# Optimization experiments

Measured on AMD Instinct MI355X. Metric: run time of the kernel, lower is better.

## Reference

```python
import jax, jax.numpy as jnp
import numpy as np

T = 2048      # tokens
H = 1024      # hidden_size
HQ = 16       # num query heads
HK = 4        # num kv heads
D = 64        # head_dim
E = 8         # num experts
K = 2         # top_k
I = 2048      # expert intermediate size
EPS = 1e-5
THETA = 10000.0


def setup_inputs() -> dict:
    key = jax.random.key(0)
    ks = jax.random.split(key, 8)
    s = 0.02
    return {
        "hidden_states": jax.random.normal(ks[0], (T, H), jnp.float32),
        "positions": jnp.arange(T, dtype=jnp.int32),
        "qkv_w": jax.random.normal(ks[1], ((HQ + 2 * HK) * D, H), jnp.float32) * s,
        "o_w": jax.random.normal(ks[2], (H, HQ * D), jnp.float32) * s,
        "norm_in_w": jnp.ones((H,), jnp.float32),
        "norm_post_w": jnp.ones((H,), jnp.float32),
        "norm_next_w": jnp.ones((H,), jnp.float32),
        "gate_w": jax.random.normal(ks[3], (E, H), jnp.float32) * s,
        "w1": jax.random.normal(ks[4], (E, I, H), jnp.float32) * s,
        "w3": jax.random.normal(ks[5], (E, I, H), jnp.float32) * s,
        "w2": jax.random.normal(ks[6], (E, H, I), jnp.float32) * s,
    }


def rmsnorm(x, w):
    var = jnp.mean(x * x, axis=-1, keepdims=True)
    return x * jax.lax.rsqrt(var + EPS) * w


def rope_neox(x, positions):
    # x: [T, nH, D]; rotate-half (neox) style
    half = D // 2
    inv_freq = 1.0 / (THETA ** (jnp.arange(0, half, dtype=jnp.float32) * 2.0 / D))
    ang = positions.astype(jnp.float32)[:, None] * inv_freq[None, :]      # [T, D/2]
    cos = jnp.cos(ang)[:, None, :]
    sin = jnp.sin(ang)[:, None, :]
    x1, x2 = x[..., :half], x[..., half:]
    return jnp.concatenate([x1 * cos - x2 * sin, x2 * cos + x1 * sin], axis=-1)


def reference(hidden_states, positions, qkv_w, o_w, norm_in_w, norm_post_w,
              norm_next_w, gate_w, w1, w3, w2):
    x = hidden_states                               # [T, H]
    residual = x
    h = rmsnorm(x, norm_in_w)                       # input_layernorm

    # ---- attention (GQA, causal, neox RoPE) ----
    qkv = h @ qkv_w.T                               # [T, (HQ+2HK)*D]
    q, k, v = jnp.split(qkv, [HQ * D, (HQ + HK) * D], axis=-1)
    q = rope_neox(q.reshape(T, HQ, D), positions)
    k = rope_neox(k.reshape(T, HK, D), positions)
    v = v.reshape(T, HK, D)
    rep = HQ // HK
    k = jnp.repeat(k, rep, axis=1)                  # [T, HQ, D]
    v = jnp.repeat(v, rep, axis=1)
    scale = D ** -0.5
    scores = jnp.einsum('qhd,khd->hqk', q, k) * scale   # [HQ, T, T]
    mask = jnp.tril(jnp.ones((T, T), dtype=bool))
    scores = jnp.where(mask[None], scores, -jnp.inf)
    probs = jax.nn.softmax(scores, axis=-1)
    attn = jnp.einsum('hqk,khd->qhd', probs, v).reshape(T, HQ * D)
    attn_out = attn @ o_w.T                         # [T, H]

    # fused allreduce(identity, world=1) + residual add + post_attention RMSNorm
    residual = residual + attn_out
    h = rmsnorm(residual, norm_post_w)

    # ---- MoE: gate, top-2, renormalize, SiLU-gated experts ----
    logits = h @ gate_w.T                           # [T, E]
    route = jax.nn.softmax(logits, axis=-1)
    topw, topi = jax.lax.top_k(route, K)            # [T, K]
    topw = topw / jnp.sum(topw, axis=-1, keepdims=True)   # renormalize
    # dense combine weights [T, E] (zero for unselected experts)
    wdense = jnp.sum(jax.nn.one_hot(topi, E, dtype=h.dtype) * topw[..., None], axis=1)
    h1 = jnp.einsum('td,eid->tei', h, w1)           # [T, E, I]
    h3 = jnp.einsum('td,eid->tei', h, w3)
    gated = jax.nn.silu(h1) * h3
    moe_out = jnp.einsum('tei,edi,te->td', gated, w2, wdense)   # [T, H]

    # fused allreduce(identity) + residual add + next layer norm
    residual = residual + moe_out
    h = rmsnorm(residual, norm_next_w)
    return h
```

## Files before the change

### kernel.cpp

```cpp
#include <hip/hip_runtime.h>
#include <hip/hip_bf16.h>
#include <math.h>

#define T_ 2048
#define H_ 1024
#define HQ_ 16
#define HK_ 4
#define D_ 64
#define NE_ 8
#define II_ 2048

typedef __attribute__((ext_vector_type(8))) short bf16x8;
typedef __attribute__((ext_vector_type(8))) unsigned short u16x8;
typedef __attribute__((ext_vector_type(4))) float f32x4;

#define GLOAD16(g, l)                                                                   \
  __builtin_amdgcn_global_load_lds((const __attribute__((address_space(1))) unsigned int*)(g), \
                                   (__attribute__((address_space(3))) unsigned int*)(l), 16, 0, 0)

__device__ __forceinline__ unsigned short f2bf(float f) {
  unsigned int u = __float_as_uint(f);
  return (unsigned short)((u + 0x7fffu + ((u >> 16) & 1u)) >> 16);
}
__device__ __forceinline__ float bf2f(unsigned short h) {
  return __uint_as_float((unsigned int)h << 16);
}

__global__ __launch_bounds__(256) void k_rmsnorm(const float* __restrict__ x, const float* __restrict__ w,
                                                 float* __restrict__ outf, unsigned short* __restrict__ outb) {
  int row = blockIdx.x;
  int tid = threadIdx.x;
  float4 v = ((const float4*)(x + (size_t)row * H_))[tid];
  float ss = v.x * v.x + v.y * v.y + v.z * v.z + v.w * v.w;
#pragma unroll
  for (int off = 32; off; off >>= 1) ss += __shfl_xor(ss, off, 64);
  __shared__ float red[4];
  int lane = tid & 63, wid = tid >> 6;
  if (lane == 0) red[wid] = ss;
  __syncthreads();
  float tot = red[0] + red[1] + red[2] + red[3];
  float inv = rsqrtf(tot * (1.0f / H_) + 1e-5f);
  float4 wv = ((const float4*)w)[tid];
  float4 o;
  o.x = v.x * inv * wv.x; o.y = v.y * inv * wv.y; o.z = v.z * inv * wv.z; o.w = v.w * inv * wv.w;
  ((float4*)(outf + (size_t)row * H_))[tid] = o;
  if (outb) {
    ushort4 b; b.x = f2bf(o.x); b.y = f2bf(o.y); b.z = f2bf(o.z); b.w = f2bf(o.w);
    ((ushort4*)(outb + (size_t)row * H_))[tid] = b;
  }
}

__global__ __launch_bounds__(256) void k_rmsnorm_split(const float* __restrict__ x, const float* __restrict__ w,
                                                       unsigned short* __restrict__ Aq) {
  int row = blockIdx.x;
  int tid = threadIdx.x;
  float4 v = ((const float4*)(x + (size_t)row * H_))[tid];
  float ss = v.x * v.x + v.y * v.y + v.z * v.z + v.w * v.w;
#pragma unroll
  for (int off = 32; off; off >>= 1) ss += __shfl_xor(ss, off, 64);
  __shared__ float red[4];
  int lane = tid & 63, wid = tid >> 6;
  if (lane == 0) red[wid] = ss;
  __syncthreads();
  float tot = red[0] + red[1] + red[2] + red[3];
  float inv = rsqrtf(tot * (1.0f / H_) + 1e-5f);
  float4 wv = ((const float4*)w)[tid];
  float4 o;
  o.x = v.x * inv * wv.x; o.y = v.y * inv * wv.y; o.z = v.z * inv * wv.z; o.w = v.w * inv * wv.w;
  ushort4 hi, lo;
  hi.x = f2bf(o.x); hi.y = f2bf(o.y); hi.z = f2bf(o.z); hi.w = f2bf(o.w);
  lo.x = f2bf(o.x - bf2f(hi.x)); lo.y = f2bf(o.y - bf2f(hi.y));
  lo.z = f2bf(o.z - bf2f(hi.z)); lo.w = f2bf(o.w - bf2f(hi.w));
  size_t base = (size_t)row * (3 * H_) + tid * 4;
  *(ushort4*)(Aq + base) = hi;
  *(ushort4*)(Aq + base + H_) = hi;
  *(ushort4*)(Aq + base + 2 * H_) = lo;
}

__global__ __launch_bounds__(256) void k_wsplit(const float* __restrict__ in, unsigned short* __restrict__ out,
                                                int K, int n8total) {
  int stride = gridDim.x * 256;
  int kc8 = K >> 3;
  for (int i = blockIdx.x * 256 + threadIdx.x; i < n8total; i += stride) {
    int n = i / kc8, kc = (i - n * kc8) * 8;
    const float4* p = (const float4*)(in + (size_t)n * K + kc);
    float4 a = p[0], b = p[1];
    u16x8 hi, lo;
    hi[0] = f2bf(a.x); hi[1] = f2bf(a.y); hi[2] = f2bf(a.z); hi[3] = f2bf(a.w);
    hi[4] = f2bf(b.x); hi[5] = f2bf(b.y); hi[6] = f2bf(b.z); hi[7] = f2bf(b.w);
    lo[0] = f2bf(a.x - bf2f(hi[0])); lo[1] = f2bf(a.y - bf2f(hi[1]));
    lo[2] = f2bf(a.z - bf2f(hi[2])); lo[3] = f2bf(a.w - bf2f(hi[3]));
    lo[4] = f2bf(b.x - bf2f(hi[4])); lo[5] = f2bf(b.y - bf2f(hi[5]));
    lo[6] = f2bf(b.z - bf2f(hi[6])); lo[7] = f2bf(b.w - bf2f(hi[7]));
    size_t ob = (size_t)n * 3 * K + kc;
    *(u16x8*)(out + ob) = hi;
    *(u16x8*)(out + ob + K) = lo;
    *(u16x8*)(out + ob + 2 * K) = hi;
  }
}

template <int ADD>
__global__ __launch_bounds__(256) void k_hgemm(const unsigned short* __restrict__ A, const unsigned short* __restrict__ B,
                                               float* __restrict__ C, const float* __restrict__ addsrc,
                                               int N, int K3) {
  int m0 = blockIdx.y * 128, n0 = blockIdx.x * 64;
  __shared__ unsigned short As[2][128 * 32];
  __shared__ unsigned short Bs[2][64 * 32];
  int tid = threadIdx.x, lane = tid & 63, w = tid >> 6;
  int wr = w >> 1, wc = w & 1;
  int l15 = lane & 15, lg = lane >> 4;
  int srow = lane >> 2, schunk = lane & 3;

  const unsigned short* ga0 = A + (size_t)(m0 + w * 32 + srow) * K3 + schunk * 8;
  const unsigned short* ga1 = A + (size_t)(m0 + w * 32 + 16 + srow) * K3 + schunk * 8;
  const unsigned short* gb = B + (size_t)(n0 + w * 16 + srow) * K3 + schunk * 8;

  f32x4 acc[4][2];
  f32x4 z = {0.f, 0.f, 0.f, 0.f};
#pragma unroll
  for (int a = 0; a < 4; a++)
#pragma unroll
    for (int b = 0; b < 2; b++) acc[a][b] = z;

  GLOAD16(ga0, &As[0][(w * 32) * 32]);
  GLOAD16(ga1, &As[0][(w * 32 + 16) * 32]);
  GLOAD16(gb, &Bs[0][(w * 16) * 32]);
  __syncthreads();

  int nt = K3 / 32;
  for (int t = 0; t < nt; ++t) {
    int cur = t & 1;
    if (t + 1 < nt) {
      int ko = (t + 1) * 32;
      GLOAD16(ga0 + ko, &As[cur ^ 1][(w * 32) * 32]);
      GLOAD16(ga1 + ko, &As[cur ^ 1][(w * 32 + 16) * 32]);
      GLOAD16(gb + ko, &Bs[cur ^ 1][(w * 16) * 32]);
    }
    bf16x8 af[4], bw2[2];
#pragma unroll
    for (int fa = 0; fa < 4; fa++)
      af[fa] = *(const bf16x8*)&As[cur][(wr * 64 + fa * 16 + l15) * 32 + lg * 8];
#pragma unroll
    for (int fb = 0; fb < 2; fb++)
      bw2[fb] = *(const bf16x8*)&Bs[cur][(wc * 32 + fb * 16 + l15) * 32 + lg * 8];
#pragma unroll
    for (int fa = 0; fa < 4; fa++)
#pragma unroll
      for (int fb = 0; fb < 2; fb++)
        acc[fa][fb] = __builtin_amdgcn_mfma_f32_16x16x32_bf16(af[fa], bw2[fb], acc[fa][fb], 0, 0, 0);
    __syncthreads();
  }
#pragma unroll
  for (int fa = 0; fa < 4; fa++)
#pragma unroll
    for (int r = 0; r < 4; r++) {
      int row = m0 + wr * 64 + fa * 16 + lg * 4 + r;
#pragma unroll
      for (int fb = 0; fb < 2; fb++) {
        int col = n0 + wc * 32 + fb * 16 + l15;
        float v = acc[fa][fb][r];
        if (ADD) v += addsrc[(size_t)row * N + col];
        C[(size_t)row * N + col] = v;
      }
    }
}

__global__ __launch_bounds__(256) void k_rope_table(const int* __restrict__ pos, float* __restrict__ ct,
                                                    float* __restrict__ st) {
  int idx = blockIdx.x * 256 + threadIdx.x;
  int t = idx >> 5, i = idx & 31;
  float p = (float)pow(10000.0, (double)i / 32.0);
  float freq = 1.0f / p;
  float ang = (float)pos[t] * freq;
  ct[idx] = cosf(ang);
  st[idx] = sinf(ang);
}

__global__ __launch_bounds__(256) void k_rope_prep(const float* __restrict__ qkv, const float* __restrict__ ct,
                                                   const float* __restrict__ st, unsigned short* __restrict__ Qhi,
                                                   unsigned short* __restrict__ Qlo, unsigned short* __restrict__ Khi,
                                                   unsigned short* __restrict__ Klo) {
  int t = blockIdx.x, tid = threadIdx.x;
  const float* row = qkv + (size_t)t * 1536;
#pragma unroll 2
  for (int it = tid; it < 512; it += 256) {
    int h = it >> 5, i = it & 31;
    float c = ct[t * 32 + i], s = st[t * 32 + i];
    float x1 = row[h * 64 + i], x2 = row[h * 64 + i + 32];
    float a = (x1 * c - x2 * s) * 0.125f;
    float b = (x2 * c + x1 * s) * 0.125f;
    size_t base = ((size_t)h * T_ + t) * 64 + i;
    unsigned short ah = f2bf(a), bh = f2bf(b);
    Qhi[base] = ah; Qhi[base + 32] = bh;
    Qlo[base] = f2bf(a - bf2f(ah));
    Qlo[base + 32] = f2bf(b - bf2f(bh));
  }
  if (tid < 128) {
    int h = tid >> 5, i = tid & 31;
    float c = ct[t * 32 + i], s = st[t * 32 + i];
    float x1 = row[1024 + h * 64 + i], x2 = row[1024 + h * 64 + i + 32];
    float a = x1 * c - x2 * s;
    float b = x2 * c + x1 * s;
    size_t base = ((size_t)h * T_ + t) * 64 + i;
    unsigned short ah = f2bf(a), bh = f2bf(b);
    Khi[base] = ah; Khi[base + 32] = bh;
    Klo[base] = f2bf(a - bf2f(ah));
    Klo[base + 32] = f2bf(b - bf2f(bh));
  }
}

__global__ __launch_bounds__(256) void k_vtrans(const float* __restrict__ qkv, unsigned short* __restrict__ Vthi,
                                                unsigned short* __restrict__ Vtlo) {
  int t0 = blockIdx.x * 64, h = blockIdx.y;
  __shared__ float tile[64][65];
  int tid = threadIdx.x;
  int c = tid & 63, w = tid >> 6;
  for (int r = w; r < 64; r += 4)
    tile[r][c] = qkv[(size_t)(t0 + r) * 1536 + 1280 + h * 64 + c];
  __syncthreads();
  for (int d = w; d < 64; d += 4) {
    float v = tile[c][d];
    unsigned short hi = f2bf(v);
    size_t idx = ((size_t)h * 64 + d) * T_ + t0 + c;
    Vthi[idx] = hi;
    Vtlo[idx] = f2bf(v - bf2f(hi));
  }
}

__global__ __launch_bounds__(256) void k_attn_mfma(const unsigned short* __restrict__ Qhi,
                                                   const unsigned short* __restrict__ Qlo,
                                                   const unsigned short* __restrict__ Khi,
                                                   const unsigned short* __restrict__ Klo,
                                                   const unsigned short* __restrict__ Vthi,
                                                   const unsigned short* __restrict__ Vtlo,
                                                   unsigned short* __restrict__ Ao) {
  int bid = blockIdx.x;
  int kk = bid >> 4;
  int head = bid & 15;
  int qidx = (kk < 16) ? (31 - kk) : (kk - 16);
  int qb = qidx * 64;
  int kvh = head >> 2;
  int tid = threadIdx.x, lane = tid & 63, w = tid >> 6;
  int l15 = lane & 15, lg = lane >> 4;

  __shared__ unsigned short KsH[64 * 72], KsL[64 * 72];
  __shared__ unsigned short VsH[64 * 72], VsL[64 * 72];
  __shared__ unsigned short PsH[64 * 72], PsL[64 * 72];

  bf16x8 qh[2], ql[2];
  {
    size_t qbase = ((size_t)head * T_ + qb + w * 16 + l15) * 64 + lg * 8;
    qh[0] = *(const bf16x8*)(Qhi + qbase);
    qh[1] = *(const bf16x8*)(Qhi + qbase + 32);
    ql[0] = *(const bf16x8*)(Qlo + qbase);
    ql[1] = *(const bf16x8*)(Qlo + qbase + 32);
  }
  f32x4 z = {0.f, 0.f, 0.f, 0.f};
  f32x4 Oa[4];
  float mrow[4], lrow[4];
#pragma unroll
  for (int r = 0; r < 4; r++) { mrow[r] = -1e30f; lrow[r] = 0.f; }
#pragma unroll
  for (int dg = 0; dg < 4; dg++) Oa[dg] = z;

  for (int jb = 0; jb <= qb; jb += 64) {
    __syncthreads();
    for (int c = tid; c < 512; c += 256) {
      int r = c >> 3, g = (c & 7) * 8;
      size_t kgl = ((size_t)kvh * T_ + jb + r) * 64 + g;
      size_t vgl = ((size_t)kvh * 64 + r) * T_ + jb + g;
      *(uint4*)&KsH[r * 72 + g] = *(const uint4*)(Khi + kgl);
      *(uint4*)&KsL[r * 72 + g] = *(const uint4*)(Klo + kgl);
      *(uint4*)&VsH[r * 72 + g] = *(const uint4*)(Vthi + vgl);
      *(uint4*)&VsL[r * 72 + g] = *(const uint4*)(Vtlo + vgl);
    }
    __syncthreads();

    f32x4 sc[4];
    sc[0] = z; sc[1] = z; sc[2] = z; sc[3] = z;
#pragma unroll
    for (int kg = 0; kg < 4; kg++) {
      int ba = (kg * 16 + l15) * 72 + lg * 8;
      bf16x8 bh0 = *(const bf16x8*)&KsH[ba];
      bf16x8 bh1 = *(const bf16x8*)&KsH[ba + 32];
      bf16x8 bl0 = *(const bf16x8*)&KsL[ba];
      bf16x8 bl1 = *(const bf16x8*)&KsL[ba + 32];
      sc[kg] = __builtin_amdgcn_mfma_f32_16x16x32_bf16(qh[0], bh0, sc[kg], 0, 0, 0);
      sc[kg] = __builtin_amdgcn_mfma_f32_16x16x32_bf16(qh[1], bh1, sc[kg], 0, 0, 0);
      sc[kg] = __builtin_amdgcn_mfma_f32_16x16x32_bf16(qh[0], bl0, sc[kg], 0, 0, 0);
      sc[kg] = __builtin_amdgcn_mfma_f32_16x16x32_bf16(qh[1], bl1, sc[kg], 0, 0, 0);
      sc[kg] = __builtin_amdgcn_mfma_f32_16x16x32_bf16(ql[0], bh0, sc[kg], 0, 0, 0);
      sc[kg] = __builtin_amdgcn_mfma_f32_16x16x32_bf16(ql[1], bh1, sc[kg], 0, 0, 0);
    }
    if (jb == qb) {
      int rb = w * 16 + lg * 4;
#pragma unroll
      for (int kg = 0; kg < 4; kg++) {
        int col = kg * 16 + l15;
#pragma unroll
        for (int r = 0; r < 4; r++)
          if (col > rb + r) sc[kg][r] = -1e30f;
      }
    }
#pragma unroll
    for (int r = 0; r < 4; r++) {
      float mt = fmaxf(fmaxf(sc[0][r], sc[1][r]), fmaxf(sc[2][r], sc[3][r]));
      mt = fmaxf(mt, __shfl_xor(mt, 1, 64));
      mt = fmaxf(mt, __shfl_xor(mt, 2, 64));
      mt = fmaxf(mt, __shfl_xor(mt, 4, 64));
      mt = fmaxf(mt, __shfl_xor(mt, 8, 64));
      float mnew = fmaxf(mrow[r], mt);
      float corr = __expf(mrow[r] - mnew);
      mrow[r] = mnew;
      float s = 0.f;
#pragma unroll
      for (int kg = 0; kg < 4; kg++) {
        float p = __expf(sc[kg][r] - mnew);
        sc[kg][r] = p;
        s += p;
      }
      s += __shfl_xor(s, 1, 64);
      s += __shfl_xor(s, 2, 64);
      s += __shfl_xor(s, 4, 64);
      s += __shfl_xor(s, 8, 64);
      lrow[r] = lrow[r] * corr + s;
#pragma unroll
      for (int dg = 0; dg < 4; dg++) Oa[dg][r] *= corr;
    }
    {
      int rb = w * 16 + lg * 4;
#pragma unroll
      for (int kg = 0; kg < 4; kg++) {
        int col = kg * 16 + l15;
#pragma unroll
        for (int r = 0; r < 4; r++) {
          float p = sc[kg][r];
          unsigned short ph = f2bf(p);
          PsH[(rb + r) * 72 + col] = ph;
          PsL[(rb + r) * 72 + col] = f2bf(p - bf2f(ph));
        }
      }
    }
    {
      int ab = (w * 16 + l15) * 72 + lg * 8;
      bf16x8 ph0 = *(const bf16x8*)&PsH[ab];
      bf16x8 ph1 = *(const bf16x8*)&PsH[ab + 32];
      bf16x8 pl0 = *(const bf16x8*)&PsL[ab];
      bf16x8 pl1 = *(const bf16x8*)&PsL[ab + 32];
#pragma unroll
      for (int dg = 0; dg < 4; dg++) {
        int vb = (dg * 16 + l15) * 72 + lg * 8;
        bf16x8 vh0 = *(const bf16x8*)&VsH[vb];
        bf16x8 vh1 = *(const bf16x8*)&VsH[vb + 32];
        bf16x8 vl0 = *(const bf16x8*)&VsL[vb];
        bf16x8 vl1 = *(const bf16x8*)&VsL[vb + 32];
        Oa[dg] = __builtin_amdgcn_mfma_f32_16x16x32_bf16(ph0, vh0, Oa[dg], 0, 0, 0);
        Oa[dg] = __builtin_amdgcn_mfma_f32_16x16x32_bf16(ph1, vh1, Oa[dg], 0, 0, 0);
        Oa[dg] = __builtin_amdgcn_mfma_f32_16x16x32_bf16(ph0, vl0, Oa[dg], 0, 0, 0);
        Oa[dg] = __builtin_amdgcn_mfma_f32_16x16x32_bf16(ph1, vl1, Oa[dg], 0, 0, 0);
        Oa[dg] = __builtin_amdgcn_mfma_f32_16x16x32_bf16(pl0, vh0, Oa[dg], 0, 0, 0);
        Oa[dg] = __builtin_amdgcn_mfma_f32_16x16x32_bf16(pl1, vh1, Oa[dg], 0, 0, 0);
      }
    }
  }
#pragma unroll
  for (int r = 0; r < 4; r++) {
    float inv = 1.0f / lrow[r];
    size_t rb2 = (size_t)(qb + w * 16 + lg * 4 + r) * 3072 + head * 64;
#pragma unroll
    for (int dg = 0; dg < 4; dg++) {
      float v = Oa[dg][r] * inv;
      unsigned short hi = f2bf(v);
      unsigned short lo = f2bf(v - bf2f(hi));
      Ao[rb2 + dg * 16 + l15] = hi;
      Ao[rb2 + 1024 + dg * 16 + l15] = hi;
      Ao[rb2 + 2048 + dg * 16 + l15] = lo;
    }
  }
}

__global__ __launch_bounds__(256) void k_router(const float* __restrict__ h2, const float* __restrict__ gw,
                                                int* __restrict__ topi, float* __restrict__ topw,
                                                int* __restrict__ counts) {
  int wid = threadIdx.x >> 6, lane = threadIdx.x & 63;
  int t = blockIdx.x * 4 + wid;
  const float* hr = h2 + (size_t)t * H_;
  float hv[16];
#pragma unroll
  for (int i = 0; i < 16; i++) hv[i] = hr[lane + 64 * i];
  float le[8];
#pragma unroll
  for (int e = 0; e < 8; e++) {
    const float* g = gw + (size_t)e * H_;
    float acc = 0.f;
#pragma unroll
    for (int i = 0; i < 16; i++) acc += hv[i] * g[lane + 64 * i];
#pragma unroll
    for (int off = 32; off; off >>= 1) acc += __shfl_xor(acc, off, 64);
    le[e] = acc;
  }
  if (lane == 0) {
    int i0 = 0;
#pragma unroll
    for (int e = 1; e < 8; e++)
      if (le[e] > le[i0]) i0 = e;
    int i1 = (i0 == 0) ? 1 : 0;
#pragma unroll
    for (int e = 0; e < 8; e++) {
      if (e == i0) continue;
      if (le[e] > le[i1]) i1 = e;
    }
    float w1r = expf(le[i1] - le[i0]);
    float denom = 1.0f + w1r;
    topi[t * 2 + 0] = i0;
    topi[t * 2 + 1] = i1;
    topw[t * 2 + 0] = 1.0f / denom;
    topw[t * 2 + 1] = w1r / denom;
    atomicAdd(&counts[i0], 1);
    atomicAdd(&counts[i1], 1);
  }
}

__global__ void k_scan(const int* __restrict__ counts, int* __restrict__ offsets) {
  if (threadIdx.x == 0 && blockIdx.x == 0) {
    int off = 0;
    for (int e = 0; e < NE_; e++) { offsets[e] = off; off += counts[e]; }
  }
}

__global__ __launch_bounds__(256) void k_build(const int* __restrict__ topi, const float* __restrict__ topw,
                                               const int* __restrict__ offsets, int* __restrict__ counts2,
                                               int* __restrict__ pairs_ts, float* __restrict__ pairs_w) {
  int t = blockIdx.x * 256 + threadIdx.x;
#pragma unroll
  for (int s = 0; s < 2; s++) {
    int e = topi[t * 2 + s];
    int slot = atomicAdd(&counts2[e], 1);
    int p = offsets[e] + slot;
    pairs_ts[p] = t * 2 + s;
    pairs_w[p] = topw[t * 2 + s];
  }
}

__global__ __launch_bounds__(256) void k_conv(const float* __restrict__ in, unsigned short* __restrict__ out, int n8) {
  int stride = gridDim.x * 256;
  for (int i = blockIdx.x * 256 + threadIdx.x; i < n8; i += stride) {
    const float4* p = (const float4*)in + (size_t)i * 2;
    float4 a = p[0], b = p[1];
    u16x8 t;
    t[0] = f2bf(a.x); t[1] = f2bf(a.y); t[2] = f2bf(a.z); t[3] = f2bf(a.w);
    t[4] = f2bf(b.x); t[5] = f2bf(b.y); t[6] = f2bf(b.z); t[7] = f2bf(b.w);
    *((u16x8*)out + i) = t;
  }
}

__global__ __launch_bounds__(256) void k_moe_up(const unsigned short* __restrict__ h2b, const unsigned short* __restrict__ W1b,
                                                const unsigned short* __restrict__ W3b, const int* __restrict__ pairs_ts,
                                                const int* __restrict__ offsets, const int* __restrict__ counts,
                                                unsigned short* __restrict__ G) {
  int e = blockIdx.z;
  int ne = counts[e];
  int row0 = blockIdx.y * 128;
  if (row0 >= ne) return;
  int col0 = blockIdx.x * 64;
  int pbase = offsets[e];
  __shared__ unsigned short As[2][128 * 32];
  __shared__ unsigned short B1s[2][64 * 32];
  __shared__ unsigned short B2s[2][64 * 32];
  int tid = threadIdx.x, lane = tid & 63, w = tid >> 6;
  int wr = w >> 1, wc = w & 1;
  int l15 = lane & 15, lg = lane >> 4;
  int srow = lane >> 2, schunk = lane & 3;

  int gr0 = row0 + w * 32 + srow, gr1 = gr0 + 16;
  int tok0 = (gr0 < ne) ? (pairs_ts[pbase + gr0] >> 1) : 0;
  int tok1 = (gr1 < ne) ? (pairs_ts[pbase + gr1] >> 1) : 0;
  const unsigned short* ga0 = h2b + (size_t)tok0 * H_ + schunk * 8;
  const unsigned short* ga1 = h2b + (size_t)tok1 * H_ + schunk * 8;
  const unsigned short* gb1 = W1b + ((size_t)e * II_ + col0 + w * 16 + srow) * H_ + schunk * 8;
  const unsigned short* gb3 = W3b + ((size_t)e * II_ + col0 + w * 16 + srow) * H_ + schunk * 8;

  f32x4 acc1[4][2], acc2[4][2];
  f32x4 z = {0.f, 0.f, 0.f, 0.f};
#pragma unroll
  for (int a = 0; a < 4; a++)
#pragma unroll
    for (int b = 0; b < 2; b++) { acc1[a][b] = z; acc2[a][b] = z; }

  GLOAD16(ga0, &As[0][(w * 32) * 32]);
  GLOAD16(ga1, &As[0][(w * 32 + 16) * 32]);
  GLOAD16(gb1, &B1s[0][(w * 16) * 32]);
  GLOAD16(gb3, &B2s[0][(w * 16) * 32]);
  __syncthreads();

  for (int t = 0; t < H_ / 32; ++t) {
    int cur = t & 1;
    if (t + 1 < H_ / 32) {
      int ko = (t + 1) * 32;
      GLOAD16(ga0 + ko, &As[cur ^ 1][(w * 32) * 32]);
      GLOAD16(ga1 + ko, &As[cur ^ 1][(w * 32 + 16) * 32]);
      GLOAD16(gb1 + ko, &B1s[cur ^ 1][(w * 16) * 32]);
      GLOAD16(gb3 + ko, &B2s[cur ^ 1][(w * 16) * 32]);
    }
    bf16x8 af[4], b1f[2], b2f[2];
#pragma unroll
    for (int fa = 0; fa < 4; fa++)
      af[fa] = *(const bf16x8*)&As[cur][(wr * 64 + fa * 16 + l15) * 32 + lg * 8];
#pragma unroll
    for (int fb = 0; fb < 2; fb++) {
      b1f[fb] = *(const bf16x8*)&B1s[cur][(wc * 32 + fb * 16 + l15) * 32 + lg * 8];
      b2f[fb] = *(const bf16x8*)&B2s[cur][(wc * 32 + fb * 16 + l15) * 32 + lg * 8];
    }
#pragma unroll
    for (int fa = 0; fa < 4; fa++)
#pragma unroll
      for (int fb = 0; fb < 2; fb++) {
        acc1[fa][fb] = __builtin_amdgcn_mfma_f32_16x16x32_bf16(af[fa], b1f[fb], acc1[fa][fb], 0, 0, 0);
        acc2[fa][fb] = __builtin_amdgcn_mfma_f32_16x16x32_bf16(af[fa], b2f[fb], acc2[fa][fb], 0, 0, 0);
      }
    __syncthreads();
  }
#pragma unroll
  for (int fa = 0; fa < 4; fa++)
#pragma unroll
    for (int r = 0; r < 4; r++) {
      int prow = row0 + wr * 64 + fa * 16 + lg * 4 + r;
      if (prow < ne) {
#pragma unroll
        for (int fb = 0; fb < 2; fb++) {
          int icol = col0 + wc * 32 + fb * 16 + l15;
          float h1 = acc1[fa][fb][r], h3 = acc2[fa][fb][r];
          float g = h1 / (1.0f + __expf(-h1)) * h3;
          G[(size_t)(pbase + prow) * II_ + icol] = f2bf(g);
        }
      }
    }
}

__global__ __launch_bounds__(256) void k_moe_down(const unsigned short* __restrict__ G, const unsigned short* __restrict__ W2b,
                                                  const int* __restrict__ pairs_ts, const float* __restrict__ pairs_w,
                                                  const int* __restrict__ offsets, const int* __restrict__ counts,
                                                  float* __restrict__ Pbuf) {
  int e = blockIdx.z;
  int ne = counts[e];
  int row0 = blockIdx.y * 128;
  if (row0 >= ne) return;
  int col0 = blockIdx.x * 64;
  int pbase = offsets[e];
  __shared__ unsigned short As[2][128 * 32];
  __shared__ unsigned short Bs[2][64 * 32];
  int tid = threadIdx.x, lane = tid & 63, w = tid >> 6;
  int wr = w >> 1, wc = w & 1;
  int l15 = lane & 15, lg = lane >> 4;
  int srow = lane >> 2, schunk = lane & 3;

  int gr0 = row0 + w * 32 + srow, gr1 = gr0 + 16;
  int p0 = pbase + ((gr0 < ne) ? gr0 : 0);
  int p1 = pbase + ((gr1 < ne) ? gr1 : 0);
  const unsigned short* ga0 = G + (size_t)p0 * II_ + schunk * 8;
  const unsigned short* ga1 = G + (size_t)p1 * II_ + schunk * 8;
  const unsigned short* gb = W2b + ((size_t)e * H_ + col0 + w * 16 + srow) * II_ + schunk * 8;

  f32x4 acc[4][2];
  f32x4 z = {0.f, 0.f, 0.f, 0.f};
#pragma unroll
  for (int a = 0; a < 4; a++)
#pragma unroll
    for (int b = 0; b < 2; b++) acc[a][b] = z;

  GLOAD16(ga0, &As[0][(w * 32) * 32]);
  GLOAD16(ga1, &As[0][(w * 32 + 16) * 32]);
  GLOAD16(gb, &Bs[0][(w * 16) * 32]);
  __syncthreads();

  for (int t = 0; t < II_ / 32; ++t) {
    int cur = t & 1;
    if (t + 1 < II_ / 32) {
      int ko = (t + 1) * 32;
      GLOAD16(ga0 + ko, &As[cur ^ 1][(w * 32) * 32]);
      GLOAD16(ga1 + ko, &As[cur ^ 1][(w * 32 + 16) * 32]);
      GLOAD16(gb + ko, &Bs[cur ^ 1][(w * 16) * 32]);
    }
    bf16x8 af[4], bw2[2];
#pragma unroll
    for (int fa = 0; fa < 4; fa++)
      af[fa] = *(const bf16x8*)&As[cur][(wr * 64 + fa * 16 + l15) * 32 + lg * 8];
#pragma unroll
    for (int fb = 0; fb < 2; fb++)
      bw2[fb] = *(const bf16x8*)&Bs[cur][(wc * 32 + fb * 16 + l15) * 32 + lg * 8];
#pragma unroll
    for (int fa = 0; fa < 4; fa++)
#pragma unroll
      for (int fb = 0; fb < 2; fb++)
        acc[fa][fb] = __builtin_amdgcn_mfma_f32_16x16x32_bf16(af[fa], bw2[fb], acc[fa][fb], 0, 0, 0);
    __syncthreads();
  }
#pragma unroll
  for (int fa = 0; fa < 4; fa++)
#pragma unroll
    for (int r = 0; r < 4; r++) {
      int prow = row0 + wr * 64 + fa * 16 + lg * 4 + r;
      if (prow < ne) {
        int p = pbase + prow;
        int ts = pairs_ts[p];
        float wgt = pairs_w[p];
#pragma unroll
        for (int fb = 0; fb < 2; fb++) {
          int col = col0 + wc * 32 + fb * 16 + l15;
          Pbuf[(size_t)ts * H_ + col] = wgt * acc[fa][fb][r];
        }
      }
    }
}

__global__ __launch_bounds__(256) void k_final(const float* __restrict__ resid, const float* __restrict__ Pbuf,
                                               const float* __restrict__ w, float* __restrict__ out) {
  int row = blockIdx.x;
  int tid = threadIdx.x;
  float4 a = ((const float4*)(resid + (size_t)row * H_))[tid];
  float4 p0 = ((const float4*)(Pbuf + (size_t)(2 * row) * H_))[tid];
  float4 p1 = ((const float4*)(Pbuf + (size_t)(2 * row + 1) * H_))[tid];
  float4 v;
  v.x = a.x + p0.x + p1.x; v.y = a.y + p0.y + p1.y; v.z = a.z + p0.z + p1.z; v.w = a.w + p0.w + p1.w;
  float ss = v.x * v.x + v.y * v.y + v.z * v.z + v.w * v.w;
#pragma unroll
  for (int off = 32; off; off >>= 1) ss += __shfl_xor(ss, off, 64);
  __shared__ float red[4];
  int lane = tid & 63, wid = tid >> 6;
  if (lane == 0) red[wid] = ss;
  __syncthreads();
  float tot = red[0] + red[1] + red[2] + red[3];
  float inv = rsqrtf(tot * (1.0f / H_) + 1e-5f);
  float4 wv = ((const float4*)w)[tid];
  float4 o;
  o.x = v.x * inv * wv.x; o.y = v.y * inv * wv.y; o.z = v.z * inv * wv.z; o.w = v.w * inv * wv.w;
  ((float4*)(out + (size_t)row * H_))[tid] = o;
}

extern "C" void kernel_launch(void* const* d_in, const int* in_sizes, int n_in,
                              void* d_out, int out_size, void* d_ws, size_t ws_size,
                              hipStream_t stream) {
  const float* x = (const float*)d_in[0];
  const int* pos = (const int*)d_in[1];
  const float* qkv_w = (const float*)d_in[2];
  const float* o_w = (const float*)d_in[3];
  const float* nin_w = (const float*)d_in[4];
  const float* npost_w = (const float*)d_in[5];
  const float* nnext_w = (const float*)d_in[6];
  const float* gate_w = (const float*)d_in[7];
  const float* w1 = (const float*)d_in[8];
  const float* w3 = (const float*)d_in[9];
  const float* w2 = (const float*)d_in[10];
  float* out = (float*)d_out;

  float* resid = (float*)d_ws;
  float* h2 = resid + (size_t)T_ * H_;
  float* Pbuf = h2 + (size_t)T_ * H_;
  float* topw = Pbuf + (size_t)2 * T_ * H_;
  float* pairsw = topw + T_ * 2;
  unsigned short* h2b = (unsigned short*)(pairsw + 4096);
  unsigned short* G = h2b + (size_t)T_ * H_;
  int* topi = (int*)(G + (size_t)2 * T_ * II_);
  int* ctrl = topi + T_ * 2;
  int* counts = ctrl;
  int* counts2 = ctrl + 8;
  int* offsets = ctrl + 16;
  int* pairs_ts = ctrl + 24;
  char* trans = (char*)(pairs_ts + 4096);
  trans = (char*)(((uintptr_t)trans + 255) & ~(uintptr_t)255);

  unsigned short* Aq = (unsigned short*)trans;
  unsigned short* Bq = Aq + (size_t)T_ * 3072;
  unsigned short* Bo = Bq + (size_t)1536 * 3072;
  unsigned short* Ao = Bo + (size_t)1024 * 3072;
  float* qkvb = (float*)(Ao + (size_t)T_ * 3072);
  float* ct = qkvb + (size_t)T_ * 1536;
  float* st = ct + (size_t)T_ * 32;
  unsigned short* uu = (unsigned short*)(st + (size_t)T_ * 32);
  unsigned short* Qhi = uu;  uu += (size_t)HQ_ * T_ * D_;
  unsigned short* Qlo = uu;  uu += (size_t)HQ_ * T_ * D_;
  unsigned short* Khi = uu;  uu += (size_t)HK_ * T_ * D_;
  unsigned short* Klo = uu;  uu += (size_t)HK_ * T_ * D_;
  unsigned short* Vthi = uu; uu += (size_t)HK_ * D_ * T_;
  unsigned short* Vtlo = uu; uu += (size_t)HK_ * D_ * T_;

  unsigned short* W1b = (unsigned short*)trans;
  unsigned short* W3b = W1b + (size_t)NE_ * II_ * H_;
  unsigned short* W2b = W3b + (size_t)NE_ * II_ * H_;

  const int WCNT8 = (NE_ * II_ * H_) / 8;

  hipMemsetAsync(ctrl, 0, 64, stream);
  k_rmsnorm_split<<<T_, 256, 0, stream>>>(x, nin_w, Aq);
  k_wsplit<<<2048, 256, 0, stream>>>(qkv_w, Bq, H_, 1536 * H_ / 8);
  k_wsplit<<<2048, 256, 0, stream>>>(o_w, Bo, HQ_ * D_, H_ * HQ_ * D_ / 8);
  k_hgemm<0><<<dim3(1536 / 64, T_ / 128), 256, 0, stream>>>(Aq, Bq, qkvb, nullptr, 1536, 3 * H_);
  k_rope_table<<<T_ * 32 / 256, 256, 0, stream>>>(pos, ct, st);
  k_rope_prep<<<T_, 256, 0, stream>>>(qkvb, ct, st, Qhi, Qlo, Khi, Klo);
  k_vtrans<<<dim3(T_ / 64, HK_), 256, 0, stream>>>(qkvb, Vthi, Vtlo);
  k_attn_mfma<<<dim3(512), 256, 0, stream>>>(Qhi, Qlo, Khi, Klo, Vthi, Vtlo, Ao);
  k_hgemm<1><<<dim3(H_ / 64, T_ / 128), 256, 0, stream>>>(Ao, Bo, resid, x, H_, 3 * HQ_ * D_);
  k_rmsnorm<<<T_, 256, 0, stream>>>(resid, npost_w, h2, h2b);
  k_router<<<T_ / 4, 256, 0, stream>>>(h2, gate_w, topi, topw, counts);
  k_scan<<<1, 64, 0, stream>>>(counts, offsets);
  k_build<<<T_ / 256, 256, 0, stream>>>(topi, topw, offsets, counts2, pairs_ts, pairsw);
  k_conv<<<2048, 256, 0, stream>>>(w1, W1b, WCNT8);
  k_conv<<<2048, 256, 0, stream>>>(w3, W3b, WCNT8);
  k_conv<<<2048, 256, 0, stream>>>(w2, W2b, WCNT8);
  k_moe_up<<<dim3(II_ / 64, T_ / 128, NE_), 256, 0, stream>>>(h2b, W1b, W3b, pairs_ts, offsets, counts, G);
  k_moe_down<<<dim3(H_ / 64, T_ / 128, NE_), 256, 0, stream>>>(G, W2b, pairs_ts, pairsw, offsets, counts, Pbuf);
  k_final<<<T_, 256, 0, stream>>>(resid, Pbuf, nnext_w, out);
}
```

Before: 489.1 us.

## Split causal attention KV range into chunks with merge kernel and register prefetch

Result: slower. 512.6 us (+4.8%).

```diff
diff --git a/kernel.cpp b/kernel.cpp
--- a/kernel.cpp
+++ b/kernel.cpp
@@ -233,12 +233,20 @@
                                                    const unsigned short* __restrict__ Klo,
                                                    const unsigned short* __restrict__ Vthi,
                                                    const unsigned short* __restrict__ Vtlo,
-                                                   unsigned short* __restrict__ Ao) {
-  int bid = blockIdx.x;
-  int kk = bid >> 4;
-  int head = bid & 15;
-  int qidx = (kk < 16) ? (31 - kk) : (kk - 16);
-  int qb = qidx * 64;
+                                                   unsigned short* __restrict__ Ao,
+                                                   float* __restrict__ Opart, float* __restrict__ mlpart) {
+  int bid = (int)gridDim.x - 1 - (int)blockIdx.x;
+  int head = bid / 80;
+  int rem = bid % 80;
+  int q, chunk;
+  if (rem < 8) { q = rem; chunk = 0; }
+  else if (rem < 24) { q = 8 + (rem - 8) / 2; chunk = (rem - 8) % 2; }
+  else if (rem < 48) { q = 16 + (rem - 24) / 3; chunk = (rem - 24) % 3; }
+  else { q = 24 + (rem - 48) / 4; chunk = (rem - 48) % 4; }
+  int nch = (q + 8) / 8;
+  int qb = q * 64;
+  int lo = chunk * 8;
+  int hi = min(lo + 8, q + 1);
   int kvh = head >> 2;
   int tid = threadIdx.x, lane = tid & 63, w = tid >> 6;
   int l15 = lane & 15, lg = lane >> 4;
@@ -263,18 +271,38 @@
 #pragma unroll
   for (int dg = 0; dg < 4; dg++) Oa[dg] = z;
 
-  for (int jb = 0; jb <= qb; jb += 64) {
+  uint4 rK[2][2], rV[2][2];
+  int sr[2], sg[2];
+#pragma unroll
+  for (int ii = 0; ii < 2; ii++) {
+    int c = tid + ii * 256;
+    sr[ii] = c >> 3;
+    sg[ii] = (c & 7) * 8;
+  }
+#define LOADREGS(jbt_)                                                              \
+  {                                                                                 \
+    int jb_ = (jbt_)*64;                                                            \
+    _Pragma("unroll") for (int ii = 0; ii < 2; ii++) {                              \
+      size_t kgl = ((size_t)kvh * T_ + jb_ + sr[ii]) * 64 + sg[ii];                 \
+      size_t vgl = ((size_t)kvh * 64 + sr[ii]) * T_ + jb_ + sg[ii];                 \
+      rK[ii][0] = *(const uint4*)(Khi + kgl);                                       \
+      rK[ii][1] = *(const uint4*)(Klo + kgl);                                       \
+      rV[ii][0] = *(const uint4*)(Vthi + vgl);                                      \
+      rV[ii][1] = *(const uint4*)(Vtlo + vgl);                                      \
+    }                                                                               \
+  }
+
+  LOADREGS(lo);
+  for (int jbt = lo; jbt < hi; ++jbt) {
+#pragma unroll
+    for (int ii = 0; ii < 2; ii++) {
+      *(uint4*)&KsH[sr[ii] * 72 + sg[ii]] = rK[ii][0];
+      *(uint4*)&KsL[sr[ii] * 72 + sg[ii]] = rK[ii][1];
+      *(uint4*)&VsH[sr[ii] * 72 + sg[ii]] = rV[ii][0];
+      *(uint4*)&VsL[sr[ii] * 72 + sg[ii]] = rV[ii][1];
+    }
     __syncthreads();
-    for (int c = tid; c < 512; c += 256) {
-      int r = c >> 3, g = (c & 7) * 8;
-      size_t kgl = ((size_t)kvh * T_ + jb + r) * 64 + g;
-      size_t vgl = ((size_t)kvh * 64 + r) * T_ + jb + g;
-      *(uint4*)&KsH[r * 72 + g] = *(const uint4*)(Khi + kgl);
-      *(uint4*)&KsL[r * 72 + g] = *(const uint4*)(Klo + kgl);
-      *(uint4*)&VsH[r * 72 + g] = *(const uint4*)(Vthi + vgl);
-      *(uint4*)&VsL[r * 72 + g] = *(const uint4*)(Vtlo + vgl);
-    }
-    __syncthreads();
+    if (jbt + 1 < hi) LOADREGS(jbt + 1);
 
     f32x4 sc[4];
     sc[0] = z; sc[1] = z; sc[2] = z; sc[3] = z;
@@ -292,7 +320,7 @@
       sc[kg] = __builtin_amdgcn_mfma_f32_16x16x32_bf16(ql[0], bh0, sc[kg], 0, 0, 0);
       sc[kg] = __builtin_amdgcn_mfma_f32_16x16x32_bf16(ql[1], bh1, sc[kg], 0, 0, 0);
     }
-    if (jb == qb) {
+    if (jbt == q) {
       int rb = w * 16 + lg * 4;
 #pragma unroll
       for (int kg = 0; kg < 4; kg++) {
@@ -362,20 +390,87 @@
         Oa[dg] = __builtin_amdgcn_mfma_f32_16x16x32_bf16(pl1, vh1, Oa[dg], 0, 0, 0);
       }
     }
-  }
-#pragma unroll
-  for (int r = 0; r < 4; r++) {
-    float inv = 1.0f / lrow[r];
-    size_t rb2 = (size_t)(qb + w * 16 + lg * 4 + r) * 3072 + head * 64;
-#pragma unroll
-    for (int dg = 0; dg < 4; dg++) {
-      float v = Oa[dg][r] * inv;
-      unsigned short hi = f2bf(v);
-      unsigned short lo = f2bf(v - bf2f(hi));
-      Ao[rb2 + dg * 16 + l15] = hi;
-      Ao[rb2 + 1024 + dg * 16 + l15] = hi;
-      Ao[rb2 + 2048 + dg * 16 + l15] = lo;
-    }
+    __syncthreads();
+  }
+
+  if (nch == 1) {
+#pragma unroll
+    for (int r = 0; r < 4; r++) {
+      float inv = 1.0f / lrow[r];
+      size_t rb2 = (size_t)(qb + w * 16 + lg * 4 + r) * 3072 + head * 64;
+#pragma unroll
+      for (int dg = 0; dg < 4; dg++) {
+        float v = Oa[dg][r] * inv;
+        unsigned short hi2 = f2bf(v);
+        unsigned short lo2 = f2bf(v - bf2f(hi2));
+        Ao[rb2 + dg * 16 + l15] = hi2;
+        Ao[rb2 + 1024 + dg * 16 + l15] = hi2;
+        Ao[rb2 + 2048 + dg * 16 + l15] = lo2;
+      }
+    }
+  } else {
+    int cidx = (head * 24 + (q - 8)) * 4 + chunk;
+#pragma unroll
+    for (int r = 0; r < 4; r++) {
+      int row = w * 16 + lg * 4 + r;
+      if (l15 == 0) {
+        mlpart[((size_t)cidx * 64 + row) * 2 + 0] = mrow[r];
+        mlpart[((size_t)cidx * 64 + row) * 2 + 1] = lrow[r];
+      }
+#pragma unroll
+      for (int dg = 0; dg < 4; dg++)
+        Opart[(size_t)cidx * 4096 + row * 64 + dg * 16 + l15] = Oa[dg][r];
+    }
+  }
+}
+
+__global__ __launch_bounds__(256) void k_attn_merge(const float* __restrict__ Opart, const float* __restrict__ mlpart,
+                                                    unsigned short* __restrict__ Ao) {
+  int q = 8 + blockIdx.x;
+  int head = blockIdx.y;
+  int nch = (q + 8) / 8;
+  int tid = threadIdx.x;
+  int r = tid >> 2, dg = tid & 3;
+  size_t cb = (size_t)(head * 24 + (q - 8)) * 4;
+  size_t obase = cb * 4096 + r * 64 + dg * 16;
+  size_t mlb = (cb * 64 + r) * 2;
+  float m[4], l[4];
+  float M = -1e30f;
+  for (int i = 0; i < nch; i++) {
+    m[i] = mlpart[mlb + i * 128];
+    l[i] = mlpart[mlb + i * 128 + 1];
+    M = fmaxf(M, m[i]);
+  }
+  float L = 0.f;
+  float sc[4];
+  for (int i = 0; i < nch; i++) {
+    sc[i] = __expf(m[i] - M);
+    L += l[i] * sc[i];
+  }
+  float invL = 1.0f / L;
+  float acc[16];
+#pragma unroll
+  for (int j = 0; j < 16; j++) acc[j] = 0.f;
+  for (int i = 0; i < nch; i++) {
+    const float4* src = (const float4*)(Opart + obase + (size_t)i * 4096);
+#pragma unroll
+    for (int j4 = 0; j4 < 4; j4++) {
+      float4 v = src[j4];
+      acc[j4 * 4 + 0] += v.x * sc[i];
+      acc[j4 * 4 + 1] += v.y * sc[i];
+      acc[j4 * 4 + 2] += v.z * sc[i];
+      acc[j4 * 4 + 3] += v.w * sc[i];
+    }
+  }
+  size_t rb2 = (size_t)(q * 64 + r) * 3072 + head * 64 + dg * 16;
+#pragma unroll
+  for (int j = 0; j < 16; j++) {
+    float v = acc[j] * invL;
+    unsigned short hi = f2bf(v);
+    unsigned short lo = f2bf(v - bf2f(hi));
+    Ao[rb2 + j] = hi;
+    Ao[rb2 + 1024 + j] = hi;
+    Ao[rb2 + 2048 + j] = lo;
   }
 }
 
@@ -684,6 +779,9 @@
   unsigned short* Vthi = uu; uu += (size_t)HK_ * D_ * T_;
   unsigned short* Vtlo = uu; uu += (size_t)HK_ * D_ * T_;
 
+  float* Opart = (float*)(Vtlo + (size_t)HK_ * D_ * T_);
+  float* mlpart = Opart + (size_t)16 * 24 * 4 * 4096;
+
   unsigned short* W1b = (unsigned short*)trans;
   unsigned short* W3b = W1b + (size_t)NE_ * II_ * H_;
   unsigned short* W2b = W3b + (size_t)NE_ * II_ * H_;
@@ -698,7 +796,8 @@
   k_rope_table<<<T_ * 32 / 256, 256, 0, stream>>>(pos, ct, st);
   k_rope_prep<<<T_, 256, 0, stream>>>(qkvb, ct, st, Qhi, Qlo, Khi, Klo);
   k_vtrans<<<dim3(T_ / 64, HK_), 256, 0, stream>>>(qkvb, Vthi, Vtlo);
-  k_attn_mfma<<<dim3(512), 256, 0, stream>>>(Qhi, Qlo, Khi, Klo, Vthi, Vtlo, Ao);
+  k_attn_mfma<<<dim3(1280), 256, 0, stream>>>(Qhi, Qlo, Khi, Klo, Vthi, Vtlo, Ao, Opart, mlpart);
+  k_attn_merge<<<dim3(24, 16), 256, 0, stream>>>(Opart, mlpart, Ao);
   k_hgemm<1><<<dim3(H_ / 64, T_ / 128), 256, 0, stream>>>(Ao, Bo, resid, x, H_, 3 * HQ_ * D_);
   k_rmsnorm<<<T_, 256, 0, stream>>>(resid, npost_w, h2, h2b);
   k_router<<<T_ / 4, 256, 0, stream>>>(h2, gate_w, topi, topw, counts);
```

## Prefetch next K/V tile into registers and alias P buffers onto K smem

Applied to the files above, without the earlier changes.

Measured after the change: 533.8 us. +9.1%, slower.

```diff
diff --git a/kernel.cpp b/kernel.cpp
--- a/kernel.cpp
+++ b/kernel.cpp
@@ -243,9 +243,13 @@
   int tid = threadIdx.x, lane = tid & 63, w = tid >> 6;
   int l15 = lane & 15, lg = lane >> 4;
 
-  __shared__ unsigned short KsH[64 * 72], KsL[64 * 72];
-  __shared__ unsigned short VsH[64 * 72], VsL[64 * 72];
-  __shared__ unsigned short PsH[64 * 72], PsL[64 * 72];
+  __shared__ unsigned short S[4 * 64 * 72];
+  unsigned short* KsH = S;
+  unsigned short* KsL = S + 4608;
+  unsigned short* VsH = S + 9216;
+  unsigned short* VsL = S + 13824;
+  unsigned short* PsH = KsH;
+  unsigned short* PsL = KsL;
 
   bf16x8 qh[2], ql[2];
   {
@@ -263,18 +267,38 @@
 #pragma unroll
   for (int dg = 0; dg < 4; dg++) Oa[dg] = z;
 
-  for (int jb = 0; jb <= qb; jb += 64) {
+  uint4 rK[2][2], rV[2][2];
+  int sr[2], sg[2];
+#pragma unroll
+  for (int ii = 0; ii < 2; ii++) {
+    int c = tid + ii * 256;
+    sr[ii] = c >> 3;
+    sg[ii] = (c & 7) * 8;
+  }
+#define LOADREGS(jbt_)                                                              \
+  {                                                                                 \
+    int jb_ = (jbt_)*64;                                                            \
+    _Pragma("unroll") for (int ii = 0; ii < 2; ii++) {                              \
+      size_t kgl = ((size_t)kvh * T_ + jb_ + sr[ii]) * 64 + sg[ii];                 \
+      size_t vgl = ((size_t)kvh * 64 + sr[ii]) * T_ + jb_ + sg[ii];                 \
+      rK[ii][0] = *(const uint4*)(Khi + kgl);                                       \
+      rK[ii][1] = *(const uint4*)(Klo + kgl);                                       \
+      rV[ii][0] = *(const uint4*)(Vthi + vgl);                                      \
+      rV[ii][1] = *(const uint4*)(Vtlo + vgl);                                      \
+    }                                                                               \
+  }
+
+  LOADREGS(0);
+  for (int jbt = 0; jbt <= qidx; ++jbt) {
+#pragma unroll
+    for (int ii = 0; ii < 2; ii++) {
+      *(uint4*)&KsH[sr[ii] * 72 + sg[ii]] = rK[ii][0];
+      *(uint4*)&KsL[sr[ii] * 72 + sg[ii]] = rK[ii][1];
+      *(uint4*)&VsH[sr[ii] * 72 + sg[ii]] = rV[ii][0];
+      *(uint4*)&VsL[sr[ii] * 72 + sg[ii]] = rV[ii][1];
+    }
     __syncthreads();
-    for (int c = tid; c < 512; c += 256) {
-      int r = c >> 3, g = (c & 7) * 8;
-      size_t kgl = ((size_t)kvh * T_ + jb + r) * 64 + g;
-      size_t vgl = ((size_t)kvh * 64 + r) * T_ + jb + g;
-      *(uint4*)&KsH[r * 72 + g] = *(const uint4*)(Khi + kgl);
-      *(uint4*)&KsL[r * 72 + g] = *(const uint4*)(Klo + kgl);
-      *(uint4*)&VsH[r * 72 + g] = *(const uint4*)(Vthi + vgl);
-      *(uint4*)&VsL[r * 72 + g] = *(const uint4*)(Vtlo + vgl);
-    }
-    __syncthreads();
+    if (jbt < qidx) LOADREGS(jbt + 1);
 
     f32x4 sc[4];
     sc[0] = z; sc[1] = z; sc[2] = z; sc[3] = z;
@@ -292,7 +316,7 @@
       sc[kg] = __builtin_amdgcn_mfma_f32_16x16x32_bf16(ql[0], bh0, sc[kg], 0, 0, 0);
       sc[kg] = __builtin_amdgcn_mfma_f32_16x16x32_bf16(ql[1], bh1, sc[kg], 0, 0, 0);
     }
-    if (jb == qb) {
+    if (jbt == qidx) {
       int rb = w * 16 + lg * 4;
 #pragma unroll
       for (int kg = 0; kg < 4; kg++) {
@@ -327,6 +351,7 @@
 #pragma unroll
       for (int dg = 0; dg < 4; dg++) Oa[dg][r] *= corr;
     }
+    __syncthreads();
     {
       int rb = w * 16 + lg * 4;
 #pragma unroll
@@ -362,6 +387,7 @@
         Oa[dg] = __builtin_amdgcn_mfma_f32_16x16x32_bf16(pl1, vh1, Oa[dg], 0, 0, 0);
       }
     }
+    __syncthreads();
   }
 #pragma unroll
   for (int r = 0; r < 4; r++) {
@@ -370,11 +396,11 @@
 #pragma unroll
     for (int dg = 0; dg < 4; dg++) {
       float v = Oa[dg][r] * inv;
-      unsigned short hi = f2bf(v);
-      unsigned short lo = f2bf(v - bf2f(hi));
-      Ao[rb2 + dg * 16 + l15] = hi;
-      Ao[rb2 + 1024 + dg * 16 + l15] = hi;
-      Ao[rb2 + 2048 + dg * 16 + l15] = lo;
+      unsigned short hi2 = f2bf(v);
+      unsigned short lo2 = f2bf(v - bf2f(hi2));
+      Ao[rb2 + dg * 16 + l15] = hi2;
+      Ao[rb2 + 1024 + dg * 16 + l15] = hi2;
+      Ao[rb2 + 2048 + dg * 16 + l15] = lo2;
     }
   }
 }
```
